# Kernel tuning notes

Hardware: AMD Instinct MI355X
Metric: run time of the kernel (lower is better)

Reference implementation:

```python
import jax, jax.numpy as jnp
import numpy as np

P, L, H = 8192, 64, 128
EPS = 1e-5


def _layer(x, W, b, g, be):
    # Linear -> LayerNorm (last dim) -> ReLU, applied to every (polyline, vector) slot.
    y = x @ W + b
    mu = jnp.mean(y, axis=-1, keepdims=True)
    var = jnp.mean((y - mu) ** 2, axis=-1, keepdims=True)
    y = (y - mu) / jnp.sqrt(var + EPS) * g + be
    return jax.nn.relu(y)


def _agg_cat(x, mask):
    # masked max over the vector dim, broadcast back and concat (the 'repeat + cat' in torch)
    phi = jnp.max(jnp.where(mask[..., None], x, -jnp.inf), axis=1, keepdims=True)  # (P,1,H)
    return jnp.concatenate([x, jnp.broadcast_to(phi, x.shape)], axis=-1)  # (P,L,2H)


def setup_inputs() -> dict:
    key = jax.random.key(0)
    ks = jax.random.split(key, 16)
    hidden_states = jax.random.normal(ks[0], (P, L, H), dtype=jnp.float32)
    lengths = jnp.maximum(jax.random.randint(ks[1], (P,), 0, L + 1), 1).astype(jnp.int32)
    s1 = 1.0 / np.sqrt(H)
    s2 = 1.0 / np.sqrt(2 * H)
    return {
        "hidden_states": hidden_states,
        "lengths": lengths,
        "W1": jax.random.normal(ks[2], (H, H), dtype=jnp.float32) * s1,
        "b1": jnp.zeros((H,), jnp.float32),
        "g1": jnp.ones((H,), jnp.float32),
        "be1": jnp.zeros((H,), jnp.float32),
        "W2": jax.random.normal(ks[3], (2 * H, H), dtype=jnp.float32) * s2,
        "b2": jnp.zeros((H,), jnp.float32),
        "g2": jnp.ones((H,), jnp.float32),
        "be2": jnp.zeros((H,), jnp.float32),
        "W3": jax.random.normal(ks[4], (2 * H, H), dtype=jnp.float32) * s2,
        "b3": jnp.zeros((H,), jnp.float32),
        "g3": jnp.ones((H,), jnp.float32),
        "be3": jnp.zeros((H,), jnp.float32),
    }


def reference(hidden_states, lengths, W1, b1, g1, be1, W2, b2, g2, be2, W3, b3, g3, be3):
    mask = jnp.arange(L)[None, :] < lengths[:, None]  # (P,L) valid-vector mask
    x = _layer(hidden_states, W1, b1, g1, be1)
    out = _agg_cat(x, mask)
    x = _layer(out, W2, b2, g2, be2)
    out = _agg_cat(x, mask)
    x = _layer(out, W3, b3, g3, be3)
    out = _agg_cat(x, mask)
    # final masked max-pool over vectors -> (P, 2H)
    poly_features = jnp.max(jnp.where(mask[..., None], out, -jnp.inf), axis=1)
    return poly_features
```

## Files before the change

### kernel.cpp

```cpp
#include <hip/hip_runtime.h>
#include <stdint.h>

#define PCNT 8192
#define LROW 64
#define HDIM 128
#define XSTR 136
#define W1STR 136
#define W23STR 264
#define W1_ELEMS (128 * W1STR)
#define W23_ELEMS (128 * W23STR)

typedef _Float16 f16;
typedef __attribute__((ext_vector_type(8))) _Float16 half8;
typedef __attribute__((ext_vector_type(4))) _Float16 half4v;
typedef __attribute__((ext_vector_type(2))) _Float16 half2v;
typedef __attribute__((ext_vector_type(4))) float f32x4;

#define MFMA16(A, B, C) __builtin_amdgcn_mfma_f32_16x16x32_f16((A), (B), (C), 0, 0, 0)

__device__ __forceinline__ half8 ldh8(const f16* p) {
  return *reinterpret_cast<const half8*>(p);
}

union PkU { uint32_t u; half2v h; };

__device__ __forceinline__ uint32_t pk2(float lo, float hi) {
  PkU a;
  a.h[0] = (f16)lo;
  a.h[1] = (f16)hi;
  return a.u;
}

__device__ __forceinline__ uint32_t pkmax(uint32_t a, uint32_t b) {
  uint32_t d;
  asm("v_pk_max_f16 %0, %1, %2" : "=v"(d) : "v"(a), "v"(b));
  return d;
}

__global__ void prep_weights(const float* __restrict__ W1,
                             const float* __restrict__ W2,
                             const float* __restrict__ W3,
                             f16* __restrict__ wt) {
  int idx = blockIdx.x * 256 + threadIdx.x;
  if (idx >= W1_ELEMS + 2 * W23_ELEMS) return;
  float v = 0.0f;
  if (idx < W1_ELEMS) {
    int c = idx / W1STR, k = idx - c * W1STR;
    if (k < 128) v = W1[k * 128 + c];
  } else {
    int rem = idx - W1_ELEMS;
    const float* W = (rem < W23_ELEMS) ? W2 : W3;
    if (rem >= W23_ELEMS) rem -= W23_ELEMS;
    int c = rem / W23STR, k = rem - c * W23STR;
    if (k < 256) v = W[k * 128 + c];
  }
  wt[idx] = (f16)v;
}

__global__ __launch_bounds__(256, 4)
void fused_subgraph(const float* __restrict__ hs,
                    const int* __restrict__ lens,
                    const f16* __restrict__ wt,
                    const float* __restrict__ b1, const float* __restrict__ g1, const float* __restrict__ be1,
                    const float* __restrict__ b2, const float* __restrict__ g2, const float* __restrict__ be2,
                    const float* __restrict__ b3, const float* __restrict__ g3, const float* __restrict__ be3,
                    float* __restrict__ out) {
  __shared__ __align__(16) f16 x_lds[LROW * XSTR];
  __shared__ __align__(16) float2 stats_s[LROW][4];
  __shared__ __align__(16) f16 phib[HDIM];

  const int tid = threadIdx.x;
  const int w = tid >> 6;
  const int l = tid & 63;
  const int p = blockIdx.x;

  int len = lens[p];
  len = (len < 1) ? 1 : (len > LROW ? LROW : len);
  const int mtiles = (len + 15) >> 4;

  const int l15 = l & 15;
  const int lg = l >> 4;
  const int ko = lg * 8;
  const int cb0 = w * 32 + lg * 4;
  const int cb1 = cb0 + 16;

  {
    const float* hp = hs + (size_t)p * (LROW * HDIM);
    for (int it = 0; it < mtiles; ++it) {
      int e = (it * 256 + tid) * 8;
      int r = e >> 7, c = e & 127;
      float4 va = *reinterpret_cast<const float4*>(hp + e);
      float4 vb = *reinterpret_cast<const float4*>(hp + e + 4);
      half8 hv;
      hv[0] = (f16)va.x; hv[1] = (f16)va.y; hv[2] = (f16)va.z; hv[3] = (f16)va.w;
      hv[4] = (f16)vb.x; hv[5] = (f16)vb.y; hv[6] = (f16)vb.z; hv[7] = (f16)vb.w;
      *reinterpret_cast<half8*>(&x_lds[r * XSTR + c]) = hv;
    }
  }
  __syncthreads();

#pragma unroll
  for (int layer = 0; layer < 3; ++layer) {
    const float* gv  = (layer == 0) ? g1  : (layer == 1) ? g2  : g3;
    const float* bev = (layer == 0) ? be1 : (layer == 1) ? be2 : be3;
    const float* bv  = (layer == 0) ? b1  : (layer == 1) ? b2  : b3;
    const f16* wa = (layer == 0) ? wt
                   : (layer == 1) ? (wt + W1_ELEMS)
                                  : (wt + W1_ELEMS + W23_ELEMS);
    const int wstr = (layer == 0) ? W1STR : W23STR;
    const int kcN  = (layer == 0) ? 4 : 8;
    const int wrow0 = (w * 32 + l15) * wstr;
    const int wrow1 = wrow0 + 16 * wstr;

    f32x4 acc[4][2];
    {
      const float4 bl0 = *reinterpret_cast<const float4*>(bv + cb0);
      const float4 bl1 = *reinterpret_cast<const float4*>(bv + cb1);
      f32x4 s0, s1;
      s0[0] = bl0.x; s0[1] = bl0.y; s0[2] = bl0.z; s0[3] = bl0.w;
      s1[0] = bl1.x; s1[1] = bl1.y; s1[2] = bl1.z; s1[3] = bl1.w;
#pragma unroll
      for (int mt = 0; mt < 4; ++mt) { acc[mt][0] = s0; acc[mt][1] = s1; }
    }
#pragma unroll
    for (int kc = 0; kc < 8; ++kc) {
      if (kc >= kcN) break;
      half8 wa0 = ldh8(&wa[wrow0 + kc * 32 + ko]);
      half8 wa1 = ldh8(&wa[wrow1 + kc * 32 + ko]);
      if (kc < 4) {
#pragma unroll
        for (int mt = 0; mt < 4; ++mt) {
          if (mt < mtiles) {
            half8 bx = ldh8(&x_lds[(mt * 16 + l15) * XSTR + kc * 32 + ko]);
            acc[mt][0] = MFMA16(wa0, bx, acc[mt][0]);
            acc[mt][1] = MFMA16(wa1, bx, acc[mt][1]);
          }
        }
      } else {
        half8 ph = ldh8(&phib[(kc - 4) * 32 + ko]);
#pragma unroll
        for (int mt = 0; mt < 4; ++mt) {
          if (mt < mtiles) {
            acc[mt][0] = MFMA16(wa0, ph, acc[mt][0]);
            acc[mt][1] = MFMA16(wa1, ph, acc[mt][1]);
          }
        }
      }
    }

#pragma unroll
    for (int mt = 0; mt < 4; ++mt) {
      if (mt < mtiles) {
        const f32x4 a0 = acc[mt][0], a1 = acc[mt][1];
        float s = ((a0[0] + a0[1]) + (a0[2] + a0[3])) + ((a1[0] + a1[1]) + (a1[2] + a1[3]));
        float q = a0[0] * a0[0];
        q = fmaf(a0[1], a0[1], q); q = fmaf(a0[2], a0[2], q); q = fmaf(a0[3], a0[3], q);
        q = fmaf(a1[0], a1[0], q); q = fmaf(a1[1], a1[1], q);
        q = fmaf(a1[2], a1[2], q); q = fmaf(a1[3], a1[3], q);
        s += __shfl_xor(s, 16); q += __shfl_xor(q, 16);
        s += __shfl_xor(s, 32); q += __shfl_xor(q, 32);
        if (l < 16) stats_s[mt * 16 + l15][w] = make_float2(s, q);
      }
    }
    __syncthreads();

    const float4 gg0 = *reinterpret_cast<const float4*>(gv + cb0);
    const float4 gg1 = *reinterpret_cast<const float4*>(gv + cb1);
    const float4 eb0 = *reinterpret_cast<const float4*>(bev + cb0);
    const float4 eb1 = *reinterpret_cast<const float4*>(bev + cb1);
    uint32_t pm[4] = {0u, 0u, 0u, 0u};
#pragma unroll
    for (int mt = 0; mt < 4; ++mt) {
      if (mt < mtiles) {
        const int row = mt * 16 + l15;
        float4 r01 = *reinterpret_cast<const float4*>(&stats_s[row][0]);
        float4 r23 = *reinterpret_cast<const float4*>(&stats_s[row][2]);
        float s = (r01.x + r01.z) + (r23.x + r23.z);
        float q = (r01.y + r01.w) + (r23.y + r23.w);
        float mu = s * (1.0f / 128.0f);
        float var = q * (1.0f / 128.0f) - mu * mu;
        float rs = rsqrtf(var + 1e-5f);
        const bool valid = row < len;
        float v0 = fmaxf((acc[mt][0][0] - mu) * rs * gg0.x + eb0.x, 0.0f);
        float v1 = fmaxf((acc[mt][0][1] - mu) * rs * gg0.y + eb0.y, 0.0f);
        float v2 = fmaxf((acc[mt][0][2] - mu) * rs * gg0.z + eb0.z, 0.0f);
        float v3 = fmaxf((acc[mt][0][3] - mu) * rs * gg0.w + eb0.w, 0.0f);
        float u0 = fmaxf((acc[mt][1][0] - mu) * rs * gg1.x + eb1.x, 0.0f);
        float u1 = fmaxf((acc[mt][1][1] - mu) * rs * gg1.y + eb1.y, 0.0f);
        float u2 = fmaxf((acc[mt][1][2] - mu) * rs * gg1.z + eb1.z, 0.0f);
        float u3 = fmaxf((acc[mt][1][3] - mu) * rs * gg1.w + eb1.w, 0.0f);
        if (layer < 2) {
          half4v h0; h0[0] = (f16)v0; h0[1] = (f16)v1; h0[2] = (f16)v2; h0[3] = (f16)v3;
          half4v h1; h1[0] = (f16)u0; h1[1] = (f16)u1; h1[2] = (f16)u2; h1[3] = (f16)u3;
          *reinterpret_cast<half4v*>(&x_lds[row * XSTR + cb0]) = h0;
          *reinterpret_cast<half4v*>(&x_lds[row * XSTR + cb1]) = h1;
        }
        pm[0] = pkmax(pm[0], pk2(valid ? v0 : 0.0f, valid ? v1 : 0.0f));
        pm[1] = pkmax(pm[1], pk2(valid ? v2 : 0.0f, valid ? v3 : 0.0f));
        pm[2] = pkmax(pm[2], pk2(valid ? u0 : 0.0f, valid ? u1 : 0.0f));
        pm[3] = pkmax(pm[3], pk2(valid ? u2 : 0.0f, valid ? u3 : 0.0f));
      }
    }
#pragma unroll
    for (int d = 1; d <= 8; d <<= 1) {
#pragma unroll
      for (int j = 0; j < 4; ++j)
        pm[j] = pkmax(pm[j], (uint32_t)__shfl_xor((int)pm[j], d));
    }

    if (layer < 2) {
      if (l15 == 0) {
        *reinterpret_cast<uint2*>(&phib[cb0]) = make_uint2(pm[0], pm[1]);
        *reinterpret_cast<uint2*>(&phib[cb1]) = make_uint2(pm[2], pm[3]);
      }
      __syncthreads();
    } else {
      if (l15 == 0) {
        PkU q0, q1, q2, q3;
        q0.u = pm[0]; q1.u = pm[1]; q2.u = pm[2]; q3.u = pm[3];
        float4 o0 = make_float4((float)q0.h[0], (float)q0.h[1], (float)q1.h[0], (float)q1.h[1]);
        float4 o1 = make_float4((float)q2.h[0], (float)q2.h[1], (float)q3.h[0], (float)q3.h[1]);
        float* op = out + (size_t)p * 256;
        *reinterpret_cast<float4*>(op + cb0) = o0;
        *reinterpret_cast<float4*>(op + cb1) = o1;
        *reinterpret_cast<float4*>(op + 128 + cb0) = o0;
        *reinterpret_cast<float4*>(op + 128 + cb1) = o1;
      }
    }
  }
}

extern "C" void kernel_launch(void* const* d_in, const int* in_sizes, int n_in,
                              void* d_out, int out_size, void* d_ws, size_t ws_size,
                              hipStream_t stream) {
  const float* hs  = (const float*)d_in[0];
  const int* lens  = (const int*)d_in[1];
  const float* W1  = (const float*)d_in[2];
  const float* b1  = (const float*)d_in[3];
  const float* g1  = (const float*)d_in[4];
  const float* be1 = (const float*)d_in[5];
  const float* W2  = (const float*)d_in[6];
  const float* b2  = (const float*)d_in[7];
  const float* g2  = (const float*)d_in[8];
  const float* be2 = (const float*)d_in[9];
  const float* W3  = (const float*)d_in[10];
  const float* b3  = (const float*)d_in[11];
  const float* g3  = (const float*)d_in[12];
  const float* be3 = (const float*)d_in[13];
  float* out = (float*)d_out;
  f16* wt = (f16*)d_ws;

  const int prep_total = W1_ELEMS + 2 * W23_ELEMS;
  prep_weights<<<(prep_total + 255) / 256, 256, 0, stream>>>(W1, W2, W3, wt);
  fused_subgraph<<<PCNT, 256, 0, stream>>>(hs, lens, wt,
                                           b1, g1, be1, b2, g2, be2, b3, g3, be3,
                                           out);
}
```

Measured before the change: 134.3 us.

## Process two polylines per block to reuse weight fragments across both

Each workgroup now handles two polylines, with separate LDS activation buffers, stats and phi buffers. Each weight fragment loaded from global memory feeds MFMAs for both polylines, halving weight traffic per polyline, and the grid shrinks to half as many blocks. In exchange accumulator registers double and LDS per block roughly doubles, which may reduce occupancy under the launch bound of 4 and lengthen the serial per-block work.

```diff
diff --git a/kernel.cpp b/kernel.cpp
--- a/kernel.cpp
+++ b/kernel.cpp
@@ -57,6 +57,21 @@
   wt[idx] = (f16)v;
 }
 
+__device__ __forceinline__ void stage_x(f16* __restrict__ x_lds,
+                                        const float* __restrict__ hp,
+                                        int mtiles, int tid) {
+  for (int it = 0; it < mtiles; ++it) {
+    int e = (it * 256 + tid) * 8;
+    int r = e >> 7, c = e & 127;
+    float4 va = *reinterpret_cast<const float4*>(hp + e);
+    float4 vb = *reinterpret_cast<const float4*>(hp + e + 4);
+    half8 hv;
+    hv[0] = (f16)va.x; hv[1] = (f16)va.y; hv[2] = (f16)va.z; hv[3] = (f16)va.w;
+    hv[4] = (f16)vb.x; hv[5] = (f16)vb.y; hv[6] = (f16)vb.z; hv[7] = (f16)vb.w;
+    *reinterpret_cast<half8*>(&x_lds[r * XSTR + c]) = hv;
+  }
+}
+
 __global__ __launch_bounds__(256, 4)
 void fused_subgraph(const float* __restrict__ hs,
                     const int* __restrict__ lens,
@@ -65,18 +80,24 @@
                     const float* __restrict__ b2, const float* __restrict__ g2, const float* __restrict__ be2,
                     const float* __restrict__ b3, const float* __restrict__ g3, const float* __restrict__ be3,
                     float* __restrict__ out) {
-  __shared__ __align__(16) f16 x_lds[LROW * XSTR];
-  __shared__ __align__(16) float2 stats_s[LROW][4];
-  __shared__ __align__(16) f16 phib[HDIM];
+  __shared__ __align__(16) f16 xA[LROW * XSTR];
+  __shared__ __align__(16) f16 xB[LROW * XSTR];
+  __shared__ __align__(16) float2 stats_s[2][LROW][4];
+  __shared__ __align__(16) f16 phiA[HDIM];
+  __shared__ __align__(16) f16 phiB[HDIM];
 
   const int tid = threadIdx.x;
   const int w = tid >> 6;
   const int l = tid & 63;
-  const int p = blockIdx.x;
-
-  int len = lens[p];
-  len = (len < 1) ? 1 : (len > LROW ? LROW : len);
-  const int mtiles = (len + 15) >> 4;
+  const int pA = blockIdx.x * 2;
+  const int pB = pA + 1;
+
+  int lenA = lens[pA];
+  lenA = (lenA < 1) ? 1 : (lenA > LROW ? LROW : lenA);
+  const int mtA = (lenA + 15) >> 4;
+  int lenB = lens[pB];
+  lenB = (lenB < 1) ? 1 : (lenB > LROW ? LROW : lenB);
+  const int mtB = (lenB + 15) >> 4;
 
   const int l15 = l & 15;
   const int lg = l >> 4;
@@ -84,19 +105,8 @@
   const int cb0 = w * 32 + lg * 4;
   const int cb1 = cb0 + 16;
 
-  {
-    const float* hp = hs + (size_t)p * (LROW * HDIM);
-    for (int it = 0; it < mtiles; ++it) {
-      int e = (it * 256 + tid) * 8;
-      int r = e >> 7, c = e & 127;
-      float4 va = *reinterpret_cast<const float4*>(hp + e);
-      float4 vb = *reinterpret_cast<const float4*>(hp + e + 4);
-      half8 hv;
-      hv[0] = (f16)va.x; hv[1] = (f16)va.y; hv[2] = (f16)va.z; hv[3] = (f16)va.w;
-      hv[4] = (f16)vb.x; hv[5] = (f16)vb.y; hv[6] = (f16)vb.z; hv[7] = (f16)vb.w;
-      *reinterpret_cast<half8*>(&x_lds[r * XSTR + c]) = hv;
-    }
-  }
+  stage_x(xA, hs + (size_t)pA * (LROW * HDIM), mtA, tid);
+  stage_x(xB, hs + (size_t)pB * (LROW * HDIM), mtB, tid);
   __syncthreads();
 
 #pragma unroll
@@ -112,7 +122,7 @@
     const int wrow0 = (w * 32 + l15) * wstr;
     const int wrow1 = wrow0 + 16 * wstr;
 
-    f32x4 acc[4][2];
+    f32x4 aA[4][2], aB[4][2];
     {
       const float4 bl0 = *reinterpret_cast<const float4*>(bv + cb0);
       const float4 bl1 = *reinterpret_cast<const float4*>(bv + cb1);
@@ -120,7 +130,10 @@
       s0[0] = bl0.x; s0[1] = bl0.y; s0[2] = bl0.z; s0[3] = bl0.w;
       s1[0] = bl1.x; s1[1] = bl1.y; s1[2] = bl1.z; s1[3] = bl1.w;
 #pragma unroll
-      for (int mt = 0; mt < 4; ++mt) { acc[mt][0] = s0; acc[mt][1] = s1; }
+      for (int mt = 0; mt < 4; ++mt) {
+        aA[mt][0] = s0; aA[mt][1] = s1;
+        aB[mt][0] = s0; aB[mt][1] = s1;
+      }
     }
 #pragma unroll
     for (int kc = 0; kc < 8; ++kc) {
@@ -130,19 +143,35 @@
       if (kc < 4) {
 #pragma unroll
         for (int mt = 0; mt < 4; ++mt) {
-          if (mt < mtiles) {
-            half8 bx = ldh8(&x_lds[(mt * 16 + l15) * XSTR + kc * 32 + ko]);
-            acc[mt][0] = MFMA16(wa0, bx, acc[mt][0]);
-            acc[mt][1] = MFMA16(wa1, bx, acc[mt][1]);
+          if (mt < mtA) {
+            half8 bx = ldh8(&xA[(mt * 16 + l15) * XSTR + kc * 32 + ko]);
+            aA[mt][0] = MFMA16(wa0, bx, aA[mt][0]);
+            aA[mt][1] = MFMA16(wa1, bx, aA[mt][1]);
+          }
+        }
+#pragma unroll
+        for (int mt = 0; mt < 4; ++mt) {
+          if (mt < mtB) {
+            half8 bx = ldh8(&xB[(mt * 16 + l15) * XSTR + kc * 32 + ko]);
+            aB[mt][0] = MFMA16(wa0, bx, aB[mt][0]);
+            aB[mt][1] = MFMA16(wa1, bx, aB[mt][1]);
           }
         }
       } else {
-        half8 ph = ldh8(&phib[(kc - 4) * 32 + ko]);
+        half8 phfA = ldh8(&phiA[(kc - 4) * 32 + ko]);
+        half8 phfB = ldh8(&phiB[(kc - 4) * 32 + ko]);
 #pragma unroll
         for (int mt = 0; mt < 4; ++mt) {
-          if (mt < mtiles) {
-            acc[mt][0] = MFMA16(wa0, ph, acc[mt][0]);
-            acc[mt][1] = MFMA16(wa1, ph, acc[mt][1]);
+          if (mt < mtA) {
+            aA[mt][0] = MFMA16(wa0, phfA, aA[mt][0]);
+            aA[mt][1] = MFMA16(wa1, phfA, aA[mt][1]);
+          }
+        }
+#pragma unroll
+        for (int mt = 0; mt < 4; ++mt) {
+          if (mt < mtB) {
+            aB[mt][0] = MFMA16(wa0, phfB, aB[mt][0]);
+            aB[mt][1] = MFMA16(wa1, phfB, aB[mt][1]);
           }
         }
       }
@@ -150,8 +179,8 @@
 
 #pragma unroll
     for (int mt = 0; mt < 4; ++mt) {
-      if (mt < mtiles) {
-        const f32x4 a0 = acc[mt][0], a1 = acc[mt][1];
+      if (mt < mtA) {
+        const f32x4 a0 = aA[mt][0], a1 = aA[mt][1];
         float s = ((a0[0] + a0[1]) + (a0[2] + a0[3])) + ((a1[0] + a1[1]) + (a1[2] + a1[3]));
         float q = a0[0] * a0[0];
         q = fmaf(a0[1], a0[1], q); q = fmaf(a0[2], a0[2], q); q = fmaf(a0[3], a0[3], q);
@@ -159,7 +188,21 @@
         q = fmaf(a1[2], a1[2], q); q = fmaf(a1[3], a1[3], q);
         s += __shfl_xor(s, 16); q += __shfl_xor(q, 16);
         s += __shfl_xor(s, 32); q += __shfl_xor(q, 32);
-        if (l < 16) stats_s[mt * 16 + l15][w] = make_float2(s, q);
+        if (l < 16) stats_s[0][mt * 16 + l15][w] = make_float2(s, q);
+      }
+    }
+#pragma unroll
+    for (int mt = 0; mt < 4; ++mt) {
+      if (mt < mtB) {
+        const f32x4 a0 = aB[mt][0], a1 = aB[mt][1];
+        float s = ((a0[0] + a0[1]) + (a0[2] + a0[3])) + ((a1[0] + a1[1]) + (a1[2] + a1[3]));
+        float q = a0[0] * a0[0];
+        q = fmaf(a0[1], a0[1], q); q = fmaf(a0[2], a0[2], q); q = fmaf(a0[3], a0[3], q);
+        q = fmaf(a1[0], a1[0], q); q = fmaf(a1[1], a1[1], q);
+        q = fmaf(a1[2], a1[2], q); q = fmaf(a1[3], a1[3], q);
+        s += __shfl_xor(s, 16); q += __shfl_xor(q, 16);
+        s += __shfl_xor(s, 32); q += __shfl_xor(q, 32);
+        if (l < 16) stats_s[1][mt * 16 + l15][w] = make_float2(s, q);
       }
     }
     __syncthreads();
@@ -168,65 +211,75 @@
     const float4 gg1 = *reinterpret_cast<const float4*>(gv + cb1);
     const float4 eb0 = *reinterpret_cast<const float4*>(bev + cb0);
     const float4 eb1 = *reinterpret_cast<const float4*>(bev + cb1);
-    uint32_t pm[4] = {0u, 0u, 0u, 0u};
-#pragma unroll
-    for (int mt = 0; mt < 4; ++mt) {
-      if (mt < mtiles) {
-        const int row = mt * 16 + l15;
-        float4 r01 = *reinterpret_cast<const float4*>(&stats_s[row][0]);
-        float4 r23 = *reinterpret_cast<const float4*>(&stats_s[row][2]);
-        float s = (r01.x + r01.z) + (r23.x + r23.z);
-        float q = (r01.y + r01.w) + (r23.y + r23.w);
-        float mu = s * (1.0f / 128.0f);
-        float var = q * (1.0f / 128.0f) - mu * mu;
-        float rs = rsqrtf(var + 1e-5f);
-        const bool valid = row < len;
-        float v0 = fmaxf((acc[mt][0][0] - mu) * rs * gg0.x + eb0.x, 0.0f);
-        float v1 = fmaxf((acc[mt][0][1] - mu) * rs * gg0.y + eb0.y, 0.0f);
-        float v2 = fmaxf((acc[mt][0][2] - mu) * rs * gg0.z + eb0.z, 0.0f);
-        float v3 = fmaxf((acc[mt][0][3] - mu) * rs * gg0.w + eb0.w, 0.0f);
-        float u0 = fmaxf((acc[mt][1][0] - mu) * rs * gg1.x + eb1.x, 0.0f);
-        float u1 = fmaxf((acc[mt][1][1] - mu) * rs * gg1.y + eb1.y, 0.0f);
-        float u2 = fmaxf((acc[mt][1][2] - mu) * rs * gg1.z + eb1.z, 0.0f);
-        float u3 = fmaxf((acc[mt][1][3] - mu) * rs * gg1.w + eb1.w, 0.0f);
-        if (layer < 2) {
-          half4v h0; h0[0] = (f16)v0; h0[1] = (f16)v1; h0[2] = (f16)v2; h0[3] = (f16)v3;
-          half4v h1; h1[0] = (f16)u0; h1[1] = (f16)u1; h1[2] = (f16)u2; h1[3] = (f16)u3;
-          *reinterpret_cast<half4v*>(&x_lds[row * XSTR + cb0]) = h0;
-          *reinterpret_cast<half4v*>(&x_lds[row * XSTR + cb1]) = h1;
-        }
-        pm[0] = pkmax(pm[0], pk2(valid ? v0 : 0.0f, valid ? v1 : 0.0f));
-        pm[1] = pkmax(pm[1], pk2(valid ? v2 : 0.0f, valid ? v3 : 0.0f));
-        pm[2] = pkmax(pm[2], pk2(valid ? u0 : 0.0f, valid ? u1 : 0.0f));
-        pm[3] = pkmax(pm[3], pk2(valid ? u2 : 0.0f, valid ? u3 : 0.0f));
-      }
-    }
-#pragma unroll
-    for (int d = 1; d <= 8; d <<= 1) {
-#pragma unroll
-      for (int j = 0; j < 4; ++j)
-        pm[j] = pkmax(pm[j], (uint32_t)__shfl_xor((int)pm[j], d));
-    }
-
-    if (layer < 2) {
-      if (l15 == 0) {
-        *reinterpret_cast<uint2*>(&phib[cb0]) = make_uint2(pm[0], pm[1]);
-        *reinterpret_cast<uint2*>(&phib[cb1]) = make_uint2(pm[2], pm[3]);
-      }
-      __syncthreads();
-    } else {
-      if (l15 == 0) {
-        PkU q0, q1, q2, q3;
-        q0.u = pm[0]; q1.u = pm[1]; q2.u = pm[2]; q3.u = pm[3];
-        float4 o0 = make_float4((float)q0.h[0], (float)q0.h[1], (float)q1.h[0], (float)q1.h[1]);
-        float4 o1 = make_float4((float)q2.h[0], (float)q2.h[1], (float)q3.h[0], (float)q3.h[1]);
-        float* op = out + (size_t)p * 256;
-        *reinterpret_cast<float4*>(op + cb0) = o0;
-        *reinterpret_cast<float4*>(op + cb1) = o1;
-        *reinterpret_cast<float4*>(op + 128 + cb0) = o0;
-        *reinterpret_cast<float4*>(op + 128 + cb1) = o1;
-      }
-    }
+
+#pragma unroll
+    for (int poly = 0; poly < 2; ++poly) {
+      const int mtP = poly ? mtB : mtA;
+      const int lenP = poly ? lenB : lenA;
+      f16* xP = poly ? xB : xA;
+      f16* phiP = poly ? phiB : phiA;
+      uint32_t pm[4] = {0u, 0u, 0u, 0u};
+#pragma unroll
+      for (int mt = 0; mt < 4; ++mt) {
+        if (mt < mtP) {
+          const f32x4 a0 = poly ? aB[mt][0] : aA[mt][0];
+          const f32x4 a1 = poly ? aB[mt][1] : aA[mt][1];
+          const int row = mt * 16 + l15;
+          float4 r01 = *reinterpret_cast<const float4*>(&stats_s[poly][row][0]);
+          float4 r23 = *reinterpret_cast<const float4*>(&stats_s[poly][row][2]);
+          float s = (r01.x + r01.z) + (r23.x + r23.z);
+          float q = (r01.y + r01.w) + (r23.y + r23.w);
+          float mu = s * (1.0f / 128.0f);
+          float var = q * (1.0f / 128.0f) - mu * mu;
+          float rs = rsqrtf(var + 1e-5f);
+          const bool valid = row < lenP;
+          float v0 = fmaxf((a0[0] - mu) * rs * gg0.x + eb0.x, 0.0f);
+          float v1 = fmaxf((a0[1] - mu) * rs * gg0.y + eb0.y, 0.0f);
+          float v2 = fmaxf((a0[2] - mu) * rs * gg0.z + eb0.z, 0.0f);
+          float v3 = fmaxf((a0[3] - mu) * rs * gg0.w + eb0.w, 0.0f);
+          float u0 = fmaxf((a1[0] - mu) * rs * gg1.x + eb1.x, 0.0f);
+          float u1 = fmaxf((a1[1] - mu) * rs * gg1.y + eb1.y, 0.0f);
+          float u2 = fmaxf((a1[2] - mu) * rs * gg1.z + eb1.z, 0.0f);
+          float u3 = fmaxf((a1[3] - mu) * rs * gg1.w + eb1.w, 0.0f);
+          if (layer < 2) {
+            half4v h0; h0[0] = (f16)v0; h0[1] = (f16)v1; h0[2] = (f16)v2; h0[3] = (f16)v3;
+            half4v h1; h1[0] = (f16)u0; h1[1] = (f16)u1; h1[2] = (f16)u2; h1[3] = (f16)u3;
+            *reinterpret_cast<half4v*>(&xP[row * XSTR + cb0]) = h0;
+            *reinterpret_cast<half4v*>(&xP[row * XSTR + cb1]) = h1;
+          }
+          pm[0] = pkmax(pm[0], pk2(valid ? v0 : 0.0f, valid ? v1 : 0.0f));
+          pm[1] = pkmax(pm[1], pk2(valid ? v2 : 0.0f, valid ? v3 : 0.0f));
+          pm[2] = pkmax(pm[2], pk2(valid ? u0 : 0.0f, valid ? u1 : 0.0f));
+          pm[3] = pkmax(pm[3], pk2(valid ? u2 : 0.0f, valid ? u3 : 0.0f));
+        }
+      }
+#pragma unroll
+      for (int d = 1; d <= 8; d <<= 1) {
+#pragma unroll
+        for (int j = 0; j < 4; ++j)
+          pm[j] = pkmax(pm[j], (uint32_t)__shfl_xor((int)pm[j], d));
+      }
+
+      if (layer < 2) {
+        if (l15 == 0) {
+          *reinterpret_cast<uint2*>(&phiP[cb0]) = make_uint2(pm[0], pm[1]);
+          *reinterpret_cast<uint2*>(&phiP[cb1]) = make_uint2(pm[2], pm[3]);
+        }
+      } else {
+        if (l15 == 0) {
+          PkU q0, q1, q2, q3;
+          q0.u = pm[0]; q1.u = pm[1]; q2.u = pm[2]; q3.u = pm[3];
+          float4 o0 = make_float4((float)q0.h[0], (float)q0.h[1], (float)q1.h[0], (float)q1.h[1]);
+          float4 o1 = make_float4((float)q2.h[0], (float)q2.h[1], (float)q3.h[0], (float)q3.h[1]);
+          float* op = out + (size_t)(poly ? pB : pA) * 256;
+          *reinterpret_cast<float4*>(op + cb0) = o0;
+          *reinterpret_cast<float4*>(op + cb1) = o1;
+          *reinterpret_cast<float4*>(op + 128 + cb0) = o0;
+          *reinterpret_cast<float4*>(op + 128 + cb1) = o1;
+        }
+      }
+    }
+    if (layer < 2) __syncthreads();
   }
 }
 
@@ -252,7 +305,7 @@
 
   const int prep_total = W1_ELEMS + 2 * W23_ELEMS;
   prep_weights<<<(prep_total + 255) / 256, 256, 0, stream>>>(W1, W2, W3, wt);
-  fused_subgraph<<<PCNT, 256, 0, stream>>>(hs, lens, wt,
-                                           b1, g1, be1, b2, g2, be2, b3, g3, be3,
-                                           out);
-}
+  fused_subgraph<<<PCNT / 2, 256, 0, stream>>>(hs, lens, wt,
+                                               b1, g1, be1, b2, g2, be2, b3, g3, be3,
+                                               out);
+}
```

Result: faster. 117.6 us (-12.4%).

## Assign one polyline per wave and drop block-level barriers

Applied to the files above, without the earlier changes.

Each wave now processes a whole polyline and computes all 128 output columns, with four polylines per block, so per-row LayerNorm statistics are reduced within the wave and no __syncthreads or shared stats buffer is needed. This removes barrier and cross-wave LDS traffic. In exchange, each wave holds four times more accumulators and loads the full weight matrix itself, which raises register pressure (launch bounds lowered to allow it) and weight load traffic.

```diff
diff --git a/kernel.cpp b/kernel.cpp
--- a/kernel.cpp
+++ b/kernel.cpp
@@ -9,6 +9,7 @@
 #define W23STR 264
 #define W1_ELEMS (128 * W1STR)
 #define W23_ELEMS (128 * W23STR)
+#define NWAVE 4
 
 typedef _Float16 f16;
 typedef __attribute__((ext_vector_type(8))) _Float16 half8;
@@ -57,7 +58,7 @@
   wt[idx] = (f16)v;
 }
 
-__global__ __launch_bounds__(256, 4)
+__global__ __launch_bounds__(256, 2)
 void fused_subgraph(const float* __restrict__ hs,
                     const int* __restrict__ lens,
                     const f16* __restrict__ wt,
@@ -65,14 +66,13 @@
                     const float* __restrict__ b2, const float* __restrict__ g2, const float* __restrict__ be2,
                     const float* __restrict__ b3, const float* __restrict__ g3, const float* __restrict__ be3,
                     float* __restrict__ out) {
-  __shared__ __align__(16) f16 x_lds[LROW * XSTR];
-  __shared__ __align__(16) float2 stats_s[LROW][4];
-  __shared__ __align__(16) f16 phib[HDIM];
+  __shared__ __align__(16) f16 x_lds[NWAVE][LROW * XSTR];
+  __shared__ __align__(16) f16 phib[NWAVE][HDIM];
 
   const int tid = threadIdx.x;
-  const int w = tid >> 6;
+  const int wv = tid >> 6;
   const int l = tid & 63;
-  const int p = blockIdx.x;
+  const int p = blockIdx.x * NWAVE + wv;
 
   int len = lens[p];
   len = (len < 1) ? 1 : (len > LROW ? LROW : len);
@@ -81,23 +81,24 @@
   const int l15 = l & 15;
   const int lg = l >> 4;
   const int ko = lg * 8;
-  const int cb0 = w * 32 + lg * 4;
-  const int cb1 = cb0 + 16;
+
+  f16* xP = x_lds[wv];
+  f16* phiP = phib[wv];
 
   {
     const float* hp = hs + (size_t)p * (LROW * HDIM);
-    for (int it = 0; it < mtiles; ++it) {
-      int e = (it * 256 + tid) * 8;
+    const int nIter = mtiles * 4;
+    for (int it = 0; it < nIter; ++it) {
+      int e = (it * 64 + l) * 8;
       int r = e >> 7, c = e & 127;
       float4 va = *reinterpret_cast<const float4*>(hp + e);
       float4 vb = *reinterpret_cast<const float4*>(hp + e + 4);
       half8 hv;
       hv[0] = (f16)va.x; hv[1] = (f16)va.y; hv[2] = (f16)va.z; hv[3] = (f16)va.w;
       hv[4] = (f16)vb.x; hv[5] = (f16)vb.y; hv[6] = (f16)vb.z; hv[7] = (f16)vb.w;
-      *reinterpret_cast<half8*>(&x_lds[r * XSTR + c]) = hv;
+      *reinterpret_cast<half8*>(&xP[r * XSTR + c]) = hv;
     }
   }
-  __syncthreads();
 
 #pragma unroll
   for (int layer = 0; layer < 3; ++layer) {
@@ -109,122 +110,121 @@
                                   : (wt + W1_ELEMS + W23_ELEMS);
     const int wstr = (layer == 0) ? W1STR : W23STR;
     const int kcN  = (layer == 0) ? 4 : 8;
-    const int wrow0 = (w * 32 + l15) * wstr;
-    const int wrow1 = wrow0 + 16 * wstr;
-
-    f32x4 acc[4][2];
-    {
-      const float4 bl0 = *reinterpret_cast<const float4*>(bv + cb0);
-      const float4 bl1 = *reinterpret_cast<const float4*>(bv + cb1);
-      f32x4 s0, s1;
-      s0[0] = bl0.x; s0[1] = bl0.y; s0[2] = bl0.z; s0[3] = bl0.w;
-      s1[0] = bl1.x; s1[1] = bl1.y; s1[2] = bl1.z; s1[3] = bl1.w;
-#pragma unroll
-      for (int mt = 0; mt < 4; ++mt) { acc[mt][0] = s0; acc[mt][1] = s1; }
+
+    f32x4 acc[4][8];
+#pragma unroll
+    for (int ct = 0; ct < 8; ++ct) {
+      const float4 bl = *reinterpret_cast<const float4*>(bv + ct * 16 + lg * 4);
+      f32x4 s;
+      s[0] = bl.x; s[1] = bl.y; s[2] = bl.z; s[3] = bl.w;
+#pragma unroll
+      for (int mt = 0; mt < 4; ++mt) acc[mt][ct] = s;
     }
 #pragma unroll
     for (int kc = 0; kc < 8; ++kc) {
       if (kc >= kcN) break;
-      half8 wa0 = ldh8(&wa[wrow0 + kc * 32 + ko]);
-      half8 wa1 = ldh8(&wa[wrow1 + kc * 32 + ko]);
+      half8 bfrag[4];
+      half8 ph;
       if (kc < 4) {
 #pragma unroll
-        for (int mt = 0; mt < 4; ++mt) {
-          if (mt < mtiles) {
-            half8 bx = ldh8(&x_lds[(mt * 16 + l15) * XSTR + kc * 32 + ko]);
-            acc[mt][0] = MFMA16(wa0, bx, acc[mt][0]);
-            acc[mt][1] = MFMA16(wa1, bx, acc[mt][1]);
-          }
-        }
+        for (int mt = 0; mt < 4; ++mt)
+          if (mt < mtiles) bfrag[mt] = ldh8(&xP[(mt * 16 + l15) * XSTR + kc * 32 + ko]);
       } else {
-        half8 ph = ldh8(&phib[(kc - 4) * 32 + ko]);
-#pragma unroll
-        for (int mt = 0; mt < 4; ++mt) {
-          if (mt < mtiles) {
-            acc[mt][0] = MFMA16(wa0, ph, acc[mt][0]);
-            acc[mt][1] = MFMA16(wa1, ph, acc[mt][1]);
-          }
-        }
-      }
-    }
-
+        ph = ldh8(&phiP[(kc - 4) * 32 + ko]);
+      }
+#pragma unroll
+      for (int ct = 0; ct < 8; ++ct) {
+        half8 wf = ldh8(&wa[(ct * 16 + l15) * wstr + kc * 32 + ko]);
+        if (kc < 4) {
+#pragma unroll
+          for (int mt = 0; mt < 4; ++mt)
+            if (mt < mtiles) acc[mt][ct] = MFMA16(wf, bfrag[mt], acc[mt][ct]);
+        } else {
+#pragma unroll
+          for (int mt = 0; mt < 4; ++mt)
+            if (mt < mtiles) acc[mt][ct] = MFMA16(wf, ph, acc[mt][ct]);
+        }
+      }
+    }
+
+    float mu_[4], rs_[4];
 #pragma unroll
     for (int mt = 0; mt < 4; ++mt) {
       if (mt < mtiles) {
-        const f32x4 a0 = acc[mt][0], a1 = acc[mt][1];
-        float s = ((a0[0] + a0[1]) + (a0[2] + a0[3])) + ((a1[0] + a1[1]) + (a1[2] + a1[3]));
-        float q = a0[0] * a0[0];
-        q = fmaf(a0[1], a0[1], q); q = fmaf(a0[2], a0[2], q); q = fmaf(a0[3], a0[3], q);
-        q = fmaf(a1[0], a1[0], q); q = fmaf(a1[1], a1[1], q);
-        q = fmaf(a1[2], a1[2], q); q = fmaf(a1[3], a1[3], q);
+        float s = 0.0f, q = 0.0f;
+#pragma unroll
+        for (int ct = 0; ct < 8; ++ct) {
+          const f32x4 a = acc[mt][ct];
+          s += (a[0] + a[1]) + (a[2] + a[3]);
+          q = fmaf(a[0], a[0], q);
+          q = fmaf(a[1], a[1], q);
+          q = fmaf(a[2], a[2], q);
+          q = fmaf(a[3], a[3], q);
+        }
         s += __shfl_xor(s, 16); q += __shfl_xor(q, 16);
         s += __shfl_xor(s, 32); q += __shfl_xor(q, 32);
-        if (l < 16) stats_s[mt * 16 + l15][w] = make_float2(s, q);
-      }
-    }
-    __syncthreads();
-
-    const float4 gg0 = *reinterpret_cast<const float4*>(gv + cb0);
-    const float4 gg1 = *reinterpret_cast<const float4*>(gv + cb1);
-    const float4 eb0 = *reinterpret_cast<const float4*>(bev + cb0);
-    const float4 eb1 = *reinterpret_cast<const float4*>(bev + cb1);
-    uint32_t pm[4] = {0u, 0u, 0u, 0u};
-#pragma unroll
-    for (int mt = 0; mt < 4; ++mt) {
-      if (mt < mtiles) {
-        const int row = mt * 16 + l15;
-        float4 r01 = *reinterpret_cast<const float4*>(&stats_s[row][0]);
-        float4 r23 = *reinterpret_cast<const float4*>(&stats_s[row][2]);
-        float s = (r01.x + r01.z) + (r23.x + r23.z);
-        float q = (r01.y + r01.w) + (r23.y + r23.w);
         float mu = s * (1.0f / 128.0f);
         float var = q * (1.0f / 128.0f) - mu * mu;
-        float rs = rsqrtf(var + 1e-5f);
-        const bool valid = row < len;
-        float v0 = fmaxf((acc[mt][0][0] - mu) * rs * gg0.x + eb0.x, 0.0f);
-        float v1 = fmaxf((acc[mt][0][1] - mu) * rs * gg0.y + eb0.y, 0.0f);
-        float v2 = fmaxf((acc[mt][0][2] - mu) * rs * gg0.z + eb0.z, 0.0f);
-        float v3 = fmaxf((acc[mt][0][3] - mu) * rs * gg0.w + eb0.w, 0.0f);
-        float u0 = fmaxf((acc[mt][1][0] - mu) * rs * gg1.x + eb1.x, 0.0f);
-        float u1 = fmaxf((acc[mt][1][1] - mu) * rs * gg1.y + eb1.y, 0.0f);
-        float u2 = fmaxf((acc[mt][1][2] - mu) * rs * gg1.z + eb1.z, 0.0f);
-        float u3 = fmaxf((acc[mt][1][3] - mu) * rs * gg1.w + eb1.w, 0.0f);
-        if (layer < 2) {
-          half4v h0; h0[0] = (f16)v0; h0[1] = (f16)v1; h0[2] = (f16)v2; h0[3] = (f16)v3;
-          half4v h1; h1[0] = (f16)u0; h1[1] = (f16)u1; h1[2] = (f16)u2; h1[3] = (f16)u3;
-          *reinterpret_cast<half4v*>(&x_lds[row * XSTR + cb0]) = h0;
-          *reinterpret_cast<half4v*>(&x_lds[row * XSTR + cb1]) = h1;
-        }
-        pm[0] = pkmax(pm[0], pk2(valid ? v0 : 0.0f, valid ? v1 : 0.0f));
-        pm[1] = pkmax(pm[1], pk2(valid ? v2 : 0.0f, valid ? v3 : 0.0f));
-        pm[2] = pkmax(pm[2], pk2(valid ? u0 : 0.0f, valid ? u1 : 0.0f));
-        pm[3] = pkmax(pm[3], pk2(valid ? u2 : 0.0f, valid ? u3 : 0.0f));
+        mu_[mt] = mu;
+        rs_[mt] = rsqrtf(var + 1e-5f);
+      }
+    }
+
+    uint32_t pm[8][2];
+#pragma unroll
+    for (int ct = 0; ct < 8; ++ct) { pm[ct][0] = 0u; pm[ct][1] = 0u; }
+#pragma unroll
+    for (int ct = 0; ct < 8; ++ct) {
+      const float4 gg = *reinterpret_cast<const float4*>(gv + ct * 16 + lg * 4);
+      const float4 eb = *reinterpret_cast<const float4*>(bev + ct * 16 + lg * 4);
+#pragma unroll
+      for (int mt = 0; mt < 4; ++mt) {
+        if (mt < mtiles) {
+          const int row = mt * 16 + l15;
+          const bool valid = row < len;
+          const float mu = mu_[mt], rs = rs_[mt];
+          float v0 = fmaxf((acc[mt][ct][0] - mu) * rs * gg.x + eb.x, 0.0f);
+          float v1 = fmaxf((acc[mt][ct][1] - mu) * rs * gg.y + eb.y, 0.0f);
+          float v2 = fmaxf((acc[mt][ct][2] - mu) * rs * gg.z + eb.z, 0.0f);
+          float v3 = fmaxf((acc[mt][ct][3] - mu) * rs * gg.w + eb.w, 0.0f);
+          if (layer < 2) {
+            half4v h;
+            h[0] = (f16)v0; h[1] = (f16)v1; h[2] = (f16)v2; h[3] = (f16)v3;
+            *reinterpret_cast<half4v*>(&xP[row * XSTR + ct * 16 + lg * 4]) = h;
+          }
+          pm[ct][0] = pkmax(pm[ct][0], pk2(valid ? v0 : 0.0f, valid ? v1 : 0.0f));
+          pm[ct][1] = pkmax(pm[ct][1], pk2(valid ? v2 : 0.0f, valid ? v3 : 0.0f));
+        }
       }
     }
 #pragma unroll
     for (int d = 1; d <= 8; d <<= 1) {
 #pragma unroll
-      for (int j = 0; j < 4; ++j)
-        pm[j] = pkmax(pm[j], (uint32_t)__shfl_xor((int)pm[j], d));
+      for (int ct = 0; ct < 8; ++ct) {
+        pm[ct][0] = pkmax(pm[ct][0], (uint32_t)__shfl_xor((int)pm[ct][0], d));
+        pm[ct][1] = pkmax(pm[ct][1], (uint32_t)__shfl_xor((int)pm[ct][1], d));
+      }
     }
 
     if (layer < 2) {
       if (l15 == 0) {
-        *reinterpret_cast<uint2*>(&phib[cb0]) = make_uint2(pm[0], pm[1]);
-        *reinterpret_cast<uint2*>(&phib[cb1]) = make_uint2(pm[2], pm[3]);
-      }
-      __syncthreads();
+#pragma unroll
+        for (int ct = 0; ct < 8; ++ct)
+          *reinterpret_cast<uint2*>(&phiP[ct * 16 + lg * 4]) =
+              make_uint2(pm[ct][0], pm[ct][1]);
+      }
     } else {
       if (l15 == 0) {
-        PkU q0, q1, q2, q3;
-        q0.u = pm[0]; q1.u = pm[1]; q2.u = pm[2]; q3.u = pm[3];
-        float4 o0 = make_float4((float)q0.h[0], (float)q0.h[1], (float)q1.h[0], (float)q1.h[1]);
-        float4 o1 = make_float4((float)q2.h[0], (float)q2.h[1], (float)q3.h[0], (float)q3.h[1]);
         float* op = out + (size_t)p * 256;
-        *reinterpret_cast<float4*>(op + cb0) = o0;
-        *reinterpret_cast<float4*>(op + cb1) = o1;
-        *reinterpret_cast<float4*>(op + 128 + cb0) = o0;
-        *reinterpret_cast<float4*>(op + 128 + cb1) = o1;
+#pragma unroll
+        for (int ct = 0; ct < 8; ++ct) {
+          PkU q0, q1;
+          q0.u = pm[ct][0]; q1.u = pm[ct][1];
+          float4 o = make_float4((float)q0.h[0], (float)q0.h[1],
+                                 (float)q1.h[0], (float)q1.h[1]);
+          *reinterpret_cast<float4*>(op + ct * 16 + lg * 4) = o;
+          *reinterpret_cast<float4*>(op + 128 + ct * 16 + lg * 4) = o;
+        }
       }
     }
   }
@@ -252,7 +252,7 @@
 
   const int prep_total = W1_ELEMS + 2 * W23_ELEMS;
   prep_weights<<<(prep_total + 255) / 256, 256, 0, stream>>>(W1, W2, W3, wt);
-  fused_subgraph<<<PCNT, 256, 0, stream>>>(hs, lens, wt,
-                                           b1, g1, be1, b2, g2, be2, b3, g3, be3,
-                                           out);
-}
+  fused_subgraph<<<PCNT / NWAVE, 256, 0, stream>>>(hs, lens, wt,
+                                                   b1, g1, be1, b2, g2, be2, b3, g3, be3,
+                                                   out);
+}
```

Measured after the change: 229.1 us. 70.5% more time.
